# Performance work log

Measured on AMD Instinct MI355X. Metric: run time of the kernel, lower is better.

## Reference

```python
import jax, jax.numpy as jnp
import numpy as np

N = 100000


def gcn_conv(x, W, b, src, dst, n):
    # PyG GCNConv (default): add self-loops, symmetric normalization,
    # linear transform then scatter-add aggregation.
    h = x @ W  # [N, out_dim]
    # self-loops
    loop = jnp.arange(n, dtype=src.dtype)
    s = jnp.concatenate([src, loop])
    d = jnp.concatenate([dst, loop])
    deg = jnp.zeros((n,), dtype=h.dtype).at[d].add(1.0)
    dinv = jnp.where(deg > 0, jax.lax.rsqrt(deg), 0.0)
    norm = dinv[s] * dinv[d]  # [E+N]
    msg = h[s] * norm[:, None]  # gather + scale
    out = jax.ops.segment_sum(msg, d, num_segments=n)  # scatter-add
    return out + b


def setup_inputs() -> dict:
    key = jax.random.key(0)
    ks = jax.random.split(key, 8)
    in_dim, h_dim, num_classes, E = 128, 128, 16, 800000
    x = jax.random.normal(ks[0], (N, in_dim), dtype=jnp.float32)
    edge_index = jax.random.randint(ks[1], (2, E), 0, N, dtype=jnp.int64)
    s1 = 1.0 / np.sqrt(in_dim)
    s2 = 1.0 / np.sqrt(h_dim)
    W1 = jax.random.uniform(ks[2], (in_dim, h_dim), jnp.float32, -s1, s1)
    b1 = jnp.zeros((h_dim,), jnp.float32)
    W2 = jax.random.uniform(ks[3], (h_dim, h_dim), jnp.float32, -s2, s2)
    b2 = jnp.zeros((h_dim,), jnp.float32)
    Wh = jax.random.uniform(ks[4], (h_dim, num_classes), jnp.float32, -s2, s2)
    bh = jax.random.uniform(ks[5], (num_classes,), jnp.float32, -s2, s2)
    return {"x": x, "W1": W1, "b1": b1, "W2": W2, "b2": b2,
            "Wh": Wh, "bh": bh, "edge_index": edge_index}


def reference(x, W1, b1, W2, b2, Wh, bh, edge_index):
    src, dst = edge_index[0], edge_index[1]
    h = gcn_conv(x, W1, b1, src, dst, N)
    h = jax.nn.relu(h)
    # dropout is identity in eval mode
    h = gcn_conv(h, W2, b2, src, dst, N)
    h = jax.nn.relu(h)
    return h @ Wh + bh  # [N, num_classes]
```

## Files before the change

kernel.cpp:

```cpp
#include <hip/hip_runtime.h>
#include <hip/hip_bf16.h>

typedef short bf16x8 __attribute__((ext_vector_type(8)));
typedef unsigned short u16x8 __attribute__((ext_vector_type(8)));
typedef float f32x4 __attribute__((ext_vector_type(4)));

#define BCAP   64
#define NBINS  256
#define EPB    2048
#define BINCAP 4096

static __device__ __forceinline__ short f2bf(float f) {
    union { float f; unsigned u; } v; v.f = f;
    unsigned r = v.u + 0x7FFF + ((v.u >> 16) & 1);
    return (short)(r >> 16);
}
static __device__ __forceinline__ float bf2f(short h) {
    union { unsigned u; float f; } v;
    v.u = ((unsigned)(unsigned short)h) << 16;
    return v.f;
}
static __device__ __forceinline__ float bfu2f(unsigned short h) {
    union { unsigned u; float f; } v;
    v.u = ((unsigned)h) << 16;
    return v.f;
}


__global__ __launch_bounds__(256) void k_pre(
    int* __restrict__ cursor,
    const float* __restrict__ W1, short* __restrict__ b1hi, short* __restrict__ b1lo,
    const float* __restrict__ W2, short* __restrict__ b2hi, short* __restrict__ b2lo,
    const float* __restrict__ Wh, short* __restrict__ whhi, short* __restrict__ whlo) {
    const int b = blockIdx.x;
    const int t = threadIdx.x;
    if (b == 0) {
        if (t < NBINS / 4) *(int4*)(cursor + t * 4) = make_int4(0, 0, 0, 0);
        return;
    }
    if (b == 17) {
        int k8 = t >> 4, c16 = t & 15, k0 = k8 * 8;
        bf16x8 h, l;
        #pragma unroll
        for (int j = 0; j < 8; ++j) {
            float v = Wh[(size_t)(k0 + j) * 16 + c16];
            short hh = f2bf(v);
            h[j] = hh;
            l[j] = f2bf(v - bf2f(hh));
        }
        *(bf16x8*)(whhi + (size_t)t * 8) = h;
        *(bf16x8*)(whlo + (size_t)t * 8) = l;
        return;
    }
    int wb = b - 1;
    const float* W = (wb < 8) ? W1 : W2;
    short* BH = (wb < 8) ? b1hi : b2hi;
    short* BL = (wb < 8) ? b1lo : b2lo;
    int u = (wb & 7) * 256 + t;
    int nb = u >> 8, k8 = (u >> 4) & 15, c16 = u & 15;
    int col = nb * 16 + c16, k0 = k8 * 8;
    bf16x8 h, l;
    #pragma unroll
    for (int j = 0; j < 8; ++j) {
        float v = W[(size_t)(k0 + j) * 128 + col];
        short hh = f2bf(v);
        h[j] = hh;
        l[j] = f2bf(v - bf2f(hh));
    }
    *(bf16x8*)(BH + (size_t)u * 8) = h;
    *(bf16x8*)(BL + (size_t)u * 8) = l;
}


template <bool F32A>
static __device__ __forceinline__ void gemm_tile_acc(
    unsigned short* As, const void* __restrict__ Aptr,
    const short* __restrict__ Bp_hi, const short* __restrict__ Bp_lo,
    int M, int m0, f32x4 (&acc)[4][4]) {
    const int tid  = threadIdx.x;
    const int wave = tid >> 6;
    const int lane = tid & 63;
    const int r16  = lane & 15;
    const int kg   = lane >> 4;
    const int mh   = (wave >> 1) * 64;
    const int nb0  = (wave & 1) * 4;

    #pragma unroll
    for (int rr = 0; rr < 8; ++rr) {
        int u = rr * 256 + tid;
        int row = u >> 4, c = u & 15;
        int rowg = m0 + row;
        if (rowg >= M) rowg = M - 1;
        bf16x8 v;
        if (F32A) {
            const float* ap = (const float*)Aptr + (size_t)rowg * 128 + c * 8;
            float4 a0 = *(const float4*)ap;
            float4 a1 = *(const float4*)(ap + 4);
            v[0] = f2bf(a0.x); v[1] = f2bf(a0.y); v[2] = f2bf(a0.z); v[3] = f2bf(a0.w);
            v[4] = f2bf(a1.x); v[5] = f2bf(a1.y); v[6] = f2bf(a1.z); v[7] = f2bf(a1.w);
        } else {
            v = *(const bf16x8*)((const unsigned short*)Aptr + (size_t)rowg * 128 + c * 8);
        }
        *(bf16x8*)(As + (size_t)(row * 16 + (c ^ (row & 7))) * 8) = v;
    }

    bf16x8 bufh[2][4], bufl[2][4];
    #pragma unroll
    for (int ni = 0; ni < 4; ++ni) {
        size_t uB = (size_t)(nb0 + ni) * 256 + (size_t)kg * 16 + r16;
        bufh[0][ni] = *(const bf16x8*)(Bp_hi + uB * 8);
        bufl[0][ni] = *(const bf16x8*)(Bp_lo + uB * 8);
    }

    __syncthreads();

    #pragma unroll
    for (int ks = 0; ks < 4; ++ks) {
        const int cur = ks & 1, nxt = cur ^ 1;
        if (ks < 3) {
            #pragma unroll
            for (int ni = 0; ni < 4; ++ni) {
                size_t uB = (size_t)(nb0 + ni) * 256 + (size_t)((ks + 1) * 4 + kg) * 16 + r16;
                bufh[nxt][ni] = *(const bf16x8*)(Bp_hi + uB * 8);
                bufl[nxt][ni] = *(const bf16x8*)(Bp_lo + uB * 8);
            }
        }
        bf16x8 a[4];
        const int c = ks * 4 + kg;
        #pragma unroll
        for (int mi = 0; mi < 4; ++mi) {
            int row = mh + mi * 16 + r16;
            a[mi] = *(const bf16x8*)(As + (size_t)(row * 16 + (c ^ (row & 7))) * 8);
        }
        #pragma unroll
        for (int mi = 0; mi < 4; ++mi)
            #pragma unroll
            for (int ni = 0; ni < 4; ++ni) {
                acc[mi][ni] = __builtin_amdgcn_mfma_f32_16x16x32_bf16(a[mi], bufl[cur][ni], acc[mi][ni], 0, 0, 0);
                acc[mi][ni] = __builtin_amdgcn_mfma_f32_16x16x32_bf16(a[mi], bufh[cur][ni], acc[mi][ni], 0, 0, 0);
            }
    }
}


__global__ __launch_bounds__(256) void k_gemm1_partA(
    const float* __restrict__ X,
    const short* __restrict__ Bp_hi, const short* __restrict__ Bp_lo,
    unsigned short* __restrict__ Cbf, int M,
    int cblocks, int total,
    const int* __restrict__ srcv, const int* __restrict__ dstv,
    int* __restrict__ cursor, int2* __restrict__ partSD,
    int E, int N) {
    __shared__ unsigned short As[128 * 128];
    const int b = blockIdx.x;
    const int lo = (int)((long long)b * cblocks / total);
    const int hi = (int)(((long long)b + 1) * cblocks / total);
    if (hi > lo) {
        int*  S       = (int*)As;
        int*  hist    = S;
        int*  incl    = S + 256;
        int*  basePos = S + 512;
        int2* stage   = (int2*)(S + 1024);
        const int t = threadIdx.x;
        hist[t] = 0;
        __syncthreads();

        const int ebase = lo * EPB + t;
        int pk[8], sv[8], dv[8];
        #pragma unroll
        for (int r = 0; r < 8; ++r) {
            int e = ebase + r * 256;
            pk[r] = -1;
            if (e < E) {
                sv[r] = srcv[e];
                dv[r] = dstv[e];
                int bin = (dv[r] * NBINS) / N;
                int rank = atomicAdd(&hist[bin], 1);
                pk[r] = (bin << 12) | rank;
            }
        }
        __syncthreads();

        const int h = hist[t];
        incl[t] = h;
        __syncthreads();
        #pragma unroll
        for (int off = 1; off < 256; off <<= 1) {
            int x = (t >= off) ? incl[t - off] : 0;
            __syncthreads();
            incl[t] += x;
            __syncthreads();
        }
        basePos[t] = atomicAdd(&cursor[t], h);
        hist[t] = incl[t] - h;
        __syncthreads();

        #pragma unroll
        for (int r = 0; r < 8; ++r) {
            if (pk[r] >= 0) {
                int bin = pk[r] >> 12;
                stage[hist[bin] + (pk[r] & 4095)] = make_int2(sv[r], dv[r]);
            }
        }
        __syncthreads();

        const int count = incl[255];
        for (int j = t; j < count; j += 256) {
            int2 sd = stage[j];
            int bin = (sd.y * NBINS) / N;
            int pos = basePos[bin] + (j - hist[bin]);
            if (pos < BINCAP) partSD[(size_t)bin * BINCAP + pos] = sd;
        }
        return;
    }

    f32x4 acc[4][4] = {};
    gemm_tile_acc<true>(As, X, Bp_hi, Bp_lo, M, (b - lo) * 128, acc);

    const int lane = threadIdx.x & 63;
    const int wave = threadIdx.x >> 6;
    const int r16  = lane & 15;
    const int m0   = (b - lo) * 128;
    const int mh   = (wave >> 1) * 64;
    const int n0   = (wave & 1) * 64;
    #pragma unroll
    for (int mi = 0; mi < 4; ++mi)
        #pragma unroll
        for (int r = 0; r < 4; ++r) {
            int row = m0 + mh + mi * 16 + (lane >> 4) * 4 + r;
            if (row < M) {
                #pragma unroll
                for (int ni = 0; ni < 4; ++ni)
                    Cbf[(size_t)row * 128 + n0 + ni * 16 + r16] =
                        (unsigned short)f2bf(acc[mi][ni][r]);
            }
        }
}


__global__ __launch_bounds__(256) void k_partB(
    const int2* __restrict__ partSD, const int* __restrict__ cursor,
    int* __restrict__ bucket, int* __restrict__ indeg, float* __restrict__ dinvA,
    int N) {
    __shared__ int cnt[400];
    const int b = blockIdx.x;
    const int t = threadIdx.x;
    const int n0 = (b * N + NBINS - 1) / NBINS;
    const int n1 = ((b + 1) * N + NBINS - 1) / NBINS;
    const int range = n1 - n0;
    for (int i = t; i < range; i += 256) cnt[i] = 0;
    __syncthreads();
    const int m = min(cursor[b], BINCAP);
    const size_t base = (size_t)b * BINCAP;
    for (int j = t; j < m; j += 256) {
        int2 sd = partSD[base + j];
        int r = atomicAdd(&cnt[sd.y - n0], 1);
        if (r < BCAP) bucket[(size_t)sd.y * BCAP + r] = sd.x;
    }
    __syncthreads();
    for (int i = t; i < range; i += 256) {
        indeg[n0 + i] = cnt[i];
        dinvA[n0 + i] = rsqrtf((float)cnt[i] + 1.0f);
    }
}


template <bool EDGEDINV, bool FINISH>
__global__ __launch_bounds__(256) void k_aggregate(const unsigned short* __restrict__ hp,
                                                   const int* __restrict__ bucket,
                                                   const int* __restrict__ indeg,
                                                   const float* __restrict__ dinvA,
                                                   const float* __restrict__ bias,
                                                   unsigned short* __restrict__ outBf, int n) {
    const int wave = (blockIdx.x * 256 + threadIdx.x) >> 6;
    const int sub  = (threadIdx.x >> 4) & 3;
    const int l16  = threadIdx.x & 15;
    const int i    = wave * 4 + sub;
    if (i >= n) return;

    const u16x8* __restrict__ h8 = (const u16x8*)hp;
    const int deg0 = indeg[i];
    const int deg  = (deg0 < BCAP) ? deg0 : BCAP;
    const float di = dinvA[i];
    const int* __restrict__ blist = bucket + (size_t)i * BCAP;

    u16x8 sv = h8[(size_t)i * 16 + l16];
    float a[8], b[8];
    #pragma unroll
    for (int q = 0; q < 8; ++q) {
        a[q] = EDGEDINV ? bfu2f(sv[q]) * di : bfu2f(sv[q]);
        b[q] = 0.f;
    }

    int j = 0;
    while (j < deg) {
        const int e1 = deg - 1;
        int   idx[4];
        float m[4];
        #pragma unroll
        for (int t = 0; t < 4; ++t) {
            int jt = j + t;
            bool ct = jt < deg;
            idx[t] = blist[ct ? jt : e1];
            m[t] = ct ? 1.f : 0.f;
        }
        if (EDGEDINV) {
            #pragma unroll
            for (int t = 0; t < 4; ++t) m[t] *= dinvA[idx[t]];
        }
        u16x8 v[4];
        #pragma unroll
        for (int t = 0; t < 4; ++t) v[t] = h8[(size_t)idx[t] * 16 + l16];
        #pragma unroll
        for (int t = 0; t < 4; t += 2) {
            #pragma unroll
            for (int q = 0; q < 8; ++q) {
                a[q] = fmaf(bfu2f(v[t][q]),     m[t],     a[q]);
                b[q] = fmaf(bfu2f(v[t + 1][q]), m[t + 1], b[q]);
            }
        }
        j += 4;
    }

    u16x8 ov;
    if (FINISH) {
        float4 bs0 = ((const float4*)bias)[l16 * 2];
        float4 bs1 = ((const float4*)bias)[l16 * 2 + 1];
        float bb[8] = {bs0.x, bs0.y, bs0.z, bs0.w, bs1.x, bs1.y, bs1.z, bs1.w};
        #pragma unroll
        for (int q = 0; q < 8; ++q) {
            float r = fmaxf(fmaf(a[q] + b[q], di, bb[q]), 0.f);
            ov[q] = (unsigned short)f2bf(r * di);
        }
    } else {
        #pragma unroll
        for (int q = 0; q < 8; ++q)
            ov[q] = (unsigned short)f2bf((a[q] + b[q]) * di);
    }
    ((u16x8*)outBf)[(size_t)i * 16 + l16] = ov;
}


__global__ __launch_bounds__(256) void k_gemm2_head(
    const unsigned short* __restrict__ T,
    const short* __restrict__ B2hi, const short* __restrict__ B2lo,
    const float* __restrict__ b2,
    const short* __restrict__ whhi, const short* __restrict__ whlo,
    const float* __restrict__ bh,
    float* __restrict__ out, int M) {
    __shared__ unsigned short As[128 * 128];
    const int tid  = threadIdx.x;
    const int wave = tid >> 6;
    const int lane = tid & 63;
    const int r16  = lane & 15;
    const int kg   = lane >> 4;
    const int m0   = blockIdx.x * 128;
    const int mh   = (wave >> 1) * 64;
    const int n0   = (wave & 1) * 64;

    f32x4 acc[4][4] = {};
    gemm_tile_acc<false>(As, T, B2hi, B2lo, M, m0, acc);

    __syncthreads();

    float b2v[4];
    #pragma unroll
    for (int ni = 0; ni < 4; ++ni) b2v[ni] = b2[n0 + ni * 16 + r16];
    #pragma unroll
    for (int mi = 0; mi < 4; ++mi)
        #pragma unroll
        for (int r = 0; r < 4; ++r) {
            int rowl = mh + mi * 16 + (lane >> 4) * 4 + r;
            #pragma unroll
            for (int ni = 0; ni < 4; ++ni) {
                int col = n0 + ni * 16 + r16;
                float u = fmaxf(acc[mi][ni][r] + b2v[ni], 0.f);
                As[(size_t)(rowl * 16 + ((col >> 3) ^ (rowl & 7))) * 8 + (col & 7)] =
                    (unsigned short)f2bf(u);
            }
        }
    __syncthreads();

    const float bhv = bh[r16];
    #pragma unroll
    for (int mt2 = 0; mt2 < 2; ++mt2) {
        const int mt = wave * 2 + mt2;
        f32x4 acc2 = {};
        #pragma unroll
        for (int ks = 0; ks < 4; ++ks) {
            const int c = ks * 4 + kg;
            const int row = mt * 16 + r16;
            bf16x8 a = *(const bf16x8*)(As + (size_t)(row * 16 + (c ^ (row & 7))) * 8);
            size_t uB = (size_t)(ks * 4 + kg) * 16 + r16;
            acc2 = __builtin_amdgcn_mfma_f32_16x16x32_bf16(a, *(const bf16x8*)(whlo + uB * 8), acc2, 0, 0, 0);
            acc2 = __builtin_amdgcn_mfma_f32_16x16x32_bf16(a, *(const bf16x8*)(whhi + uB * 8), acc2, 0, 0, 0);
        }
        #pragma unroll
        for (int r = 0; r < 4; ++r) {
            int row = m0 + mt * 16 + (lane >> 4) * 4 + r;
            if (row < M) out[(size_t)row * 16 + r16] = acc2[r] + bhv;
        }
    }
}


extern "C" void kernel_launch(void* const* d_in, const int* in_sizes, int n_in,
                              void* d_out, int out_size, void* d_ws, size_t ws_size,
                              hipStream_t stream) {
    const float* x  = (const float*)d_in[0];
    const float* W1 = (const float*)d_in[1];
    const float* b1 = (const float*)d_in[2];
    const float* W2 = (const float*)d_in[3];
    const float* b2 = (const float*)d_in[4];
    const float* Wh = (const float*)d_in[5];
    const float* bh = (const float*)d_in[6];
    const int*   ei = (const int*)d_in[7];

    const int N = in_sizes[0] / 128;
    const int E = in_sizes[7] / 2;
    const int* src = ei;
    const int* dst = ei + E;
    float* out = (float*)d_out;

    char* w = (char*)d_ws;
    auto alloc = [&](size_t bytes) -> void* {
        void* p = (void*)w;
        w += (bytes + 255) & ~(size_t)255;
        return p;
    };
    unsigned short* hp     = (unsigned short*)alloc((size_t)N * 128 * sizeof(short));
    unsigned short* actB   = (unsigned short*)alloc((size_t)N * 128 * sizeof(short));
    int*   indeg  = (int*)alloc((size_t)N * sizeof(int));
    float* dinvA  = (float*)alloc((size_t)N * sizeof(float));
    int*   bucket = (int*)alloc((size_t)N * BCAP * sizeof(int));
    int*   cursor = (int*)alloc((size_t)NBINS * sizeof(int));
    int2*  partSD = (int2*)alloc((size_t)NBINS * BINCAP * sizeof(int2));
    short* w1hiP  = (short*)alloc(128 * 128 * sizeof(short));
    short* w1loP  = (short*)alloc(128 * 128 * sizeof(short));
    short* w2hiP  = (short*)alloc(128 * 128 * sizeof(short));
    short* w2loP  = (short*)alloc(128 * 128 * sizeof(short));
    short* whhiP  = (short*)alloc(128 * 16 * sizeof(short));
    short* whloP  = (short*)alloc(128 * 16 * sizeof(short));

    const int gblocks = (N + 127) / 128;
    const int ablocks = (N + 15) / 16;
    const int cblocks = (E + EPB - 1) / EPB;
    const int total   = gblocks + cblocks;

    k_pre<<<18, 256, 0, stream>>>(cursor, W1, w1hiP, w1loP, W2, w2hiP, w2loP,
                                  Wh, whhiP, whloP);
    k_gemm1_partA<<<total, 256, 0, stream>>>(x, w1hiP, w1loP, hp, N,
                                             cblocks, total, src, dst,
                                             cursor, partSD, E, N);
    k_partB<<<NBINS, 256, 0, stream>>>(partSD, cursor, bucket, indeg, dinvA, N);
    k_aggregate<true, true><<<ablocks, 256, 0, stream>>>(hp, bucket, indeg, dinvA,
                                                         b1, actB, N);
    k_aggregate<false, false><<<ablocks, 256, 0, stream>>>(actB, bucket, indeg, dinvA,
                                                           nullptr, hp, N);
    k_gemm2_head<<<gblocks, 256, 0, stream>>>(hp, w2hiP, w2loP, b2,
                                              whhiP, whloP, bh, out, N);
}
```

Before: 132.9 us.

## Fuse second-layer aggregation into GEMM2+head kernel via shared-memory tile

The second aggregation kernel is removed. Each GEMM2 block now gathers neighbor rows for its 128 nodes directly and writes the normalized bf16 result into the swizzled LDS A-tile, which the MFMA loop then consumes. This drops one kernel launch and the write and re-read of the intermediate 100k x 128 bf16 buffer. The cost is that the gather runs inside GEMM blocks, which have lower occupancy (32KB LDS each) and fewer blocks (782 versus 6250), so latency hiding for the random gathers may suffer.

```diff
diff --git a/kernel.cpp b/kernel.cpp
--- a/kernel.cpp
+++ b/kernel.cpp
@@ -72,11 +72,10 @@
 }
 
 
-template <bool F32A>
-static __device__ __forceinline__ void gemm_tile_acc(
-    unsigned short* As, const void* __restrict__ Aptr,
+static __device__ __forceinline__ void mfma_loop(
+    const unsigned short* As,
     const short* __restrict__ Bp_hi, const short* __restrict__ Bp_lo,
-    int M, int m0, f32x4 (&acc)[4][4]) {
+    f32x4 (&acc)[4][4]) {
     const int tid  = threadIdx.x;
     const int wave = tid >> 6;
     const int lane = tid & 63;
@@ -85,6 +84,50 @@
     const int mh   = (wave >> 1) * 64;
     const int nb0  = (wave & 1) * 4;
 
+    bf16x8 bufh[2][4], bufl[2][4];
+    #pragma unroll
+    for (int ni = 0; ni < 4; ++ni) {
+        size_t uB = (size_t)(nb0 + ni) * 256 + (size_t)kg * 16 + r16;
+        bufh[0][ni] = *(const bf16x8*)(Bp_hi + uB * 8);
+        bufl[0][ni] = *(const bf16x8*)(Bp_lo + uB * 8);
+    }
+
+    __syncthreads();
+
+    #pragma unroll
+    for (int ks = 0; ks < 4; ++ks) {
+        const int cur = ks & 1, nxt = cur ^ 1;
+        if (ks < 3) {
+            #pragma unroll
+            for (int ni = 0; ni < 4; ++ni) {
+                size_t uB = (size_t)(nb0 + ni) * 256 + (size_t)((ks + 1) * 4 + kg) * 16 + r16;
+                bufh[nxt][ni] = *(const bf16x8*)(Bp_hi + uB * 8);
+                bufl[nxt][ni] = *(const bf16x8*)(Bp_lo + uB * 8);
+            }
+        }
+        bf16x8 a[4];
+        const int c = ks * 4 + kg;
+        #pragma unroll
+        for (int mi = 0; mi < 4; ++mi) {
+            int row = mh + mi * 16 + r16;
+            a[mi] = *(const bf16x8*)(As + (size_t)(row * 16 + (c ^ (row & 7))) * 8);
+        }
+        #pragma unroll
+        for (int mi = 0; mi < 4; ++mi)
+            #pragma unroll
+            for (int ni = 0; ni < 4; ++ni) {
+                acc[mi][ni] = __builtin_amdgcn_mfma_f32_16x16x32_bf16(a[mi], bufl[cur][ni], acc[mi][ni], 0, 0, 0);
+                acc[mi][ni] = __builtin_amdgcn_mfma_f32_16x16x32_bf16(a[mi], bufh[cur][ni], acc[mi][ni], 0, 0, 0);
+            }
+    }
+}
+
+template <bool F32A>
+static __device__ __forceinline__ void gemm_tile_acc(
+    unsigned short* As, const void* __restrict__ Aptr,
+    const short* __restrict__ Bp_hi, const short* __restrict__ Bp_lo,
+    int M, int m0, f32x4 (&acc)[4][4]) {
+    const int tid = threadIdx.x;
     #pragma unroll
     for (int rr = 0; rr < 8; ++rr) {
         int u = rr * 256 + tid;
@@ -103,43 +146,7 @@
         }
         *(bf16x8*)(As + (size_t)(row * 16 + (c ^ (row & 7))) * 8) = v;
     }
-
-    bf16x8 bufh[2][4], bufl[2][4];
-    #pragma unroll
-    for (int ni = 0; ni < 4; ++ni) {
-        size_t uB = (size_t)(nb0 + ni) * 256 + (size_t)kg * 16 + r16;
-        bufh[0][ni] = *(const bf16x8*)(Bp_hi + uB * 8);
-        bufl[0][ni] = *(const bf16x8*)(Bp_lo + uB * 8);
-    }
-
-    __syncthreads();
-
-    #pragma unroll
-    for (int ks = 0; ks < 4; ++ks) {
-        const int cur = ks & 1, nxt = cur ^ 1;
-        if (ks < 3) {
-            #pragma unroll
-            for (int ni = 0; ni < 4; ++ni) {
-                size_t uB = (size_t)(nb0 + ni) * 256 + (size_t)((ks + 1) * 4 + kg) * 16 + r16;
-                bufh[nxt][ni] = *(const bf16x8*)(Bp_hi + uB * 8);
-                bufl[nxt][ni] = *(const bf16x8*)(Bp_lo + uB * 8);
-            }
-        }
-        bf16x8 a[4];
-        const int c = ks * 4 + kg;
-        #pragma unroll
-        for (int mi = 0; mi < 4; ++mi) {
-            int row = mh + mi * 16 + r16;
-            a[mi] = *(const bf16x8*)(As + (size_t)(row * 16 + (c ^ (row & 7))) * 8);
-        }
-        #pragma unroll
-        for (int mi = 0; mi < 4; ++mi)
-            #pragma unroll
-            for (int ni = 0; ni < 4; ++ni) {
-                acc[mi][ni] = __builtin_amdgcn_mfma_f32_16x16x32_bf16(a[mi], bufl[cur][ni], acc[mi][ni], 0, 0, 0);
-                acc[mi][ni] = __builtin_amdgcn_mfma_f32_16x16x32_bf16(a[mi], bufh[cur][ni], acc[mi][ni], 0, 0, 0);
-            }
-    }
+    mfma_loop(As, Bp_hi, Bp_lo, acc);
 }
 
 
@@ -265,13 +272,13 @@
 }
 
 
-template <bool EDGEDINV, bool FINISH>
-__global__ __launch_bounds__(256) void k_aggregate(const unsigned short* __restrict__ hp,
-                                                   const int* __restrict__ bucket,
-                                                   const int* __restrict__ indeg,
-                                                   const float* __restrict__ dinvA,
-                                                   const float* __restrict__ bias,
-                                                   unsigned short* __restrict__ outBf, int n) {
+__global__ __launch_bounds__(256) void k_aggregate1(const unsigned short* __restrict__ hp,
+                                                    const int* __restrict__ bucket,
+                                                    const int* __restrict__ indeg,
+                                                    const float* __restrict__ dinvA,
+                                                    const float* __restrict__ bias,
+                                                    unsigned short* __restrict__ outBf,
+                                                    int n) {
     const int wave = (blockIdx.x * 256 + threadIdx.x) >> 6;
     const int sub  = (threadIdx.x >> 4) & 3;
     const int l16  = threadIdx.x & 15;
@@ -287,10 +294,7 @@
     u16x8 sv = h8[(size_t)i * 16 + l16];
     float a[8], b[8];
     #pragma unroll
-    for (int q = 0; q < 8; ++q) {
-        a[q] = EDGEDINV ? bfu2f(sv[q]) * di : bfu2f(sv[q]);
-        b[q] = 0.f;
-    }
+    for (int q = 0; q < 8; ++q) { a[q] = bfu2f(sv[q]) * di; b[q] = 0.f; }
 
     int j = 0;
     while (j < deg) {
@@ -304,10 +308,8 @@
             idx[t] = blist[ct ? jt : e1];
             m[t] = ct ? 1.f : 0.f;
         }
-        if (EDGEDINV) {
-            #pragma unroll
-            for (int t = 0; t < 4; ++t) m[t] *= dinvA[idx[t]];
-        }
+        #pragma unroll
+        for (int t = 0; t < 4; ++t) m[t] *= dinvA[idx[t]];
         u16x8 v[4];
         #pragma unroll
         for (int t = 0; t < 4; ++t) v[t] = h8[(size_t)idx[t] * 16 + l16];
@@ -322,27 +324,23 @@
         j += 4;
     }
 
+    float4 bs0 = ((const float4*)bias)[l16 * 2];
+    float4 bs1 = ((const float4*)bias)[l16 * 2 + 1];
+    float bb[8] = {bs0.x, bs0.y, bs0.z, bs0.w, bs1.x, bs1.y, bs1.z, bs1.w};
     u16x8 ov;
-    if (FINISH) {
-        float4 bs0 = ((const float4*)bias)[l16 * 2];
-        float4 bs1 = ((const float4*)bias)[l16 * 2 + 1];
-        float bb[8] = {bs0.x, bs0.y, bs0.z, bs0.w, bs1.x, bs1.y, bs1.z, bs1.w};
-        #pragma unroll
-        for (int q = 0; q < 8; ++q) {
-            float r = fmaxf(fmaf(a[q] + b[q], di, bb[q]), 0.f);
-            ov[q] = (unsigned short)f2bf(r * di);
-        }
-    } else {
-        #pragma unroll
-        for (int q = 0; q < 8; ++q)
-            ov[q] = (unsigned short)f2bf((a[q] + b[q]) * di);
+    #pragma unroll
+    for (int q = 0; q < 8; ++q) {
+        float r = fmaxf(fmaf(a[q] + b[q], di, bb[q]), 0.f);
+        ov[q] = (unsigned short)f2bf(r * di);
     }
     ((u16x8*)outBf)[(size_t)i * 16 + l16] = ov;
 }
 
 
-__global__ __launch_bounds__(256) void k_gemm2_head(
-    const unsigned short* __restrict__ T,
+__global__ __launch_bounds__(256) void k_agg2_gemm_head(
+    const unsigned short* __restrict__ Sbf,
+    const int* __restrict__ bucket, const int* __restrict__ indeg,
+    const float* __restrict__ dinvA,
     const short* __restrict__ B2hi, const short* __restrict__ B2lo,
     const float* __restrict__ b2,
     const short* __restrict__ whhi, const short* __restrict__ whlo,
@@ -354,15 +352,64 @@
     const int lane = tid & 63;
     const int r16  = lane & 15;
     const int kg   = lane >> 4;
+    const int sub  = (tid >> 4) & 3;
+    const int l16  = tid & 15;
     const int m0   = blockIdx.x * 128;
-    const int mh   = (wave >> 1) * 64;
-    const int n0   = (wave & 1) * 64;
+
+    const u16x8* __restrict__ s8 = (const u16x8*)Sbf;
+    #pragma unroll 2
+    for (int iter = 0; iter < 8; ++iter) {
+        const int iloc = iter * 16 + wave * 4 + sub;
+        const int i = m0 + iloc;
+        u16x8 ov = {};
+        if (i < M) {
+            const int deg0 = indeg[i];
+            const int deg  = (deg0 < BCAP) ? deg0 : BCAP;
+            const float di = dinvA[i];
+            const int* __restrict__ blist = bucket + (size_t)i * BCAP;
+            u16x8 sv = s8[(size_t)i * 16 + l16];
+            float a[8], b[8];
+            #pragma unroll
+            for (int q = 0; q < 8; ++q) { a[q] = bfu2f(sv[q]); b[q] = 0.f; }
+            int j = 0;
+            while (j < deg) {
+                const int e1 = deg - 1;
+                int   idx[4];
+                float m[4];
+                #pragma unroll
+                for (int t = 0; t < 4; ++t) {
+                    int jt = j + t;
+                    bool ct = jt < deg;
+                    idx[t] = blist[ct ? jt : e1];
+                    m[t] = ct ? 1.f : 0.f;
+                }
+                u16x8 v[4];
+                #pragma unroll
+                for (int t = 0; t < 4; ++t) v[t] = s8[(size_t)idx[t] * 16 + l16];
+                #pragma unroll
+                for (int t = 0; t < 4; t += 2) {
+                    #pragma unroll
+                    for (int q = 0; q < 8; ++q) {
+                        a[q] = fmaf(bfu2f(v[t][q]),     m[t],     a[q]);
+                        b[q] = fmaf(bfu2f(v[t + 1][q]), m[t + 1], b[q]);
+                    }
+                }
+                j += 4;
+            }
+            #pragma unroll
+            for (int q = 0; q < 8; ++q)
+                ov[q] = (unsigned short)f2bf((a[q] + b[q]) * di);
+        }
+        *(u16x8*)(As + (size_t)(iloc * 16 + (l16 ^ (iloc & 7))) * 8) = ov;
+    }
 
     f32x4 acc[4][4] = {};
-    gemm_tile_acc<false>(As, T, B2hi, B2lo, M, m0, acc);
+    mfma_loop(As, B2hi, B2lo, acc);
 
     __syncthreads();
 
+    const int mh = (wave >> 1) * 64;
+    const int n0 = (wave & 1) * 64;
     float b2v[4];
     #pragma unroll
     for (int ni = 0; ni < 4; ++ni) b2v[ni] = b2[n0 + ni * 16 + r16];
@@ -453,10 +500,8 @@
                                              cblocks, total, src, dst,
                                              cursor, partSD, E, N);
     k_partB<<<NBINS, 256, 0, stream>>>(partSD, cursor, bucket, indeg, dinvA, N);
-    k_aggregate<true, true><<<ablocks, 256, 0, stream>>>(hp, bucket, indeg, dinvA,
-                                                         b1, actB, N);
-    k_aggregate<false, false><<<ablocks, 256, 0, stream>>>(actB, bucket, indeg, dinvA,
-                                                           nullptr, hp, N);
-    k_gemm2_head<<<gblocks, 256, 0, stream>>>(hp, w2hiP, w2loP, b2,
-                                              whhiP, whloP, bh, out, N);
-}
+    k_aggregate1<<<ablocks, 256, 0, stream>>>(hp, bucket, indeg, dinvA, b1, actB, N);
+    k_agg2_gemm_head<<<gblocks, 256, 0, stream>>>(actB, bucket, indeg, dinvA,
+                                                  w2hiP, w2loP, b2,
+                                                  whhiP, whloP, bh, out, N);
+}
```

New measurement: 143.6 us. 1.08x slower.
